# Kernel tuning notes

Measured on AMD Instinct MI355X. Metric: run time of the kernel, lower is better.

Reference implementation:

```python
import jax, jax.numpy as jnp
import numpy as np

TOTAL = 16384
IN_DIM = 512
OUT_DIM = 512
HEADS = 8
NUM_GRAPHS = 16


def setup_inputs() -> dict:
    key = jax.random.key(0)
    ks = jax.random.split(key, 8)
    x = jax.random.normal(ks[0], (TOTAL, IN_DIM), dtype=jnp.float32)
    batch = jnp.sort(jax.random.randint(ks[1], (TOTAL,), 0, NUM_GRAPHS)).astype(jnp.int64)
    s = 0.02
    # torch nn.MultiheadAttention packed in-projection: [3E, E] weight, [3E] bias
    in_proj_w = jax.random.normal(ks[2], (3 * IN_DIM, IN_DIM), dtype=jnp.float32) * s
    in_proj_b = jnp.zeros((3 * IN_DIM,), dtype=jnp.float32)
    out_proj_w = jax.random.normal(ks[3], (IN_DIM, IN_DIM), dtype=jnp.float32) * s
    out_proj_b = jnp.zeros((IN_DIM,), dtype=jnp.float32)
    lin_w = jax.random.normal(ks[4], (OUT_DIM, IN_DIM), dtype=jnp.float32) * s
    lin_b = jnp.zeros((OUT_DIM,), dtype=jnp.float32)
    return {"x": x, "batch": batch, "in_proj_w": in_proj_w, "in_proj_b": in_proj_b,
            "out_proj_w": out_proj_w, "out_proj_b": out_proj_b,
            "lin_w": lin_w, "lin_b": lin_b}


def _dense_indices(batch):
    """Host-side computation of (B, max_len, pos) from the sorted segment ids."""
    b_np = np.asarray(batch)
    B = int(b_np.max()) + 1
    counts = np.bincount(b_np, minlength=B)
    max_len = int(counts.max())
    offsets = np.concatenate([[0], np.cumsum(counts)[:-1]])  # start of each graph
    pos = jnp.asarray(np.arange(b_np.shape[0]) - offsets[b_np])  # within-graph index
    return B, max_len, pos


def reference(x, batch, in_proj_w, in_proj_b, out_proj_w, out_proj_b, lin_w, lin_b):
    T, E = x.shape
    H = HEADS
    D = E // H
    B, N, pos = _dense_indices(batch)

    # to_dense_batch: scatter ragged tokens into [B, N, E] + boolean mask [B, N]
    x_dense = jnp.zeros((B, N, E), x.dtype).at[batch, pos].set(x)
    mask = jnp.zeros((B, N), bool).at[batch, pos].set(True)

    # packed in-projection (torch MultiheadAttention semantics)
    qkv = x_dense @ in_proj_w.T + in_proj_b            # [B, N, 3E]
    q, k, v = jnp.split(qkv, 3, axis=-1)
    q = q.reshape(B, N, H, D)
    k = k.reshape(B, N, H, D)
    v = v.reshape(B, N, H, D)

    scores = jnp.einsum('bqhd,bkhd->bhqk', q, k) / jnp.sqrt(jnp.float32(D))
    # key_padding_mask = ~mask: padded keys are excluded
    scores = jnp.where(mask[:, None, None, :], scores, -jnp.inf)
    attn = jax.nn.softmax(scores, axis=-1)             # [B, H, N, N]
    ctx = jnp.einsum('bhqk,bkhd->bqhd', attn, v).reshape(B, N, E)
    attn_out = ctx @ out_proj_w.T + out_proj_b         # [B, N, E]

    y_dense = attn_out @ lin_w.T + lin_b               # [B, N, OUT_DIM]
    # unpad: x_out = y_dense[mask] == gather at the same (batch, pos) indices
    return y_dense[batch, pos]
```

## Files before the change

### kernel.cpp

```cpp
#include <hip/hip_runtime.h>
#include <stdint.h>
#include <stddef.h>

typedef unsigned short u16;
typedef unsigned int u32;
typedef __bf16 bf16x8 __attribute__((ext_vector_type(8)));
typedef _Float16 f16x8 __attribute__((ext_vector_type(8)));
typedef float f32x4 __attribute__((ext_vector_type(4)));

#define TT 16384
#define NG 16
#define MAXT 160
#define SCL 0.18033688011112042f

static __device__ __forceinline__ unsigned f2bf_u(float f) {
  unsigned u = __float_as_uint(f);
  return (u + 0x7fffu + ((u >> 16) & 1u)) >> 16;
}

static __device__ __forceinline__ void gl_lds16(const u16* g, u16* l) {
  __builtin_amdgcn_global_load_lds(
      (const __attribute__((address_space(1))) u32*)g,
      (__attribute__((address_space(3))) u32*)l, 16, 0, 0);
}

template <int CTRL>
static __device__ __forceinline__ float dppf(float x) {
  return __int_as_float(__builtin_amdgcn_mov_dpp(__float_as_int(x), CTRL, 0xF, 0xF, true));
}

#define NXF4 2097152
#define NWQ4 65536

__global__ __launch_bounds__(256) void prep_wc_kernel(
    const float* __restrict__ x, const float* __restrict__ ipw,
    const int* __restrict__ batch, const float* __restrict__ ipb,
    u16* __restrict__ xb, u16* __restrict__ ipwb, float* __restrict__ bqk,
    int* __restrict__ seg,
    const float* __restrict__ Wl, const float* __restrict__ Wo,
    const float* __restrict__ bo, const float* __restrict__ bl,
    u16* __restrict__ Wc, float* __restrict__ bc) {
  const int tid = threadIdx.x;
  __shared__ float sWl[16][512];
  __shared__ float red[256];
  __shared__ int scnt[NG];
  if (blockIdx.x > 1120) {
    const int bw = blockIdx.x - 1121;
    const int r0 = (bw >> 2) << 4;
    const int c0 = (bw & 3) << 7;
    const int col = c0 + (tid & 127), rh = (tid >> 7) << 3;
    for (int i = tid; i < 16 * 512; i += 256)
      sWl[i >> 9][i & 511] = Wl[(r0 + (i >> 9)) * 512 + (i & 511)];
    __syncthreads();
    float a[8] = {};
#pragma unroll 4
    for (int k = 0; k < 512; ++k) {
      float w = Wo[k * 512 + col];
#pragma unroll
      for (int r = 0; r < 8; ++r) a[r] += sWl[rh + r][k] * w;
    }
#pragma unroll
    for (int r = 0; r < 8; ++r) Wc[(r0 + rh + r) * 512 + col] = (u16)f2bf_u(a[r]);
    if (c0 == 0) {
      for (int r = 0; r < 16; ++r) {
        float p = 0.f;
        for (int k = tid; k < 512; k += 256) p += sWl[r][k] * bo[k];
        red[tid] = p;
        __syncthreads();
        for (int st = 128; st > 0; st >>= 1) {
          if (tid < st) red[tid] += red[tid + st];
          __syncthreads();
        }
        if (tid == 0) bc[r0 + r] = red[0] + bl[r0 + r];
        __syncthreads();
      }
    }
    return;
  }
  if (blockIdx.x == 1120) {
    if (tid < NG) scnt[tid] = 0;
    __syncthreads();
    for (int i = tid; i < TT; i += 256) atomicAdd(&scnt[batch[i] & (NG - 1)], 1);
    for (int i = tid; i < 1024; i += 256) bqk[i] = ipb[i] * (i < 512 ? SCL : 1.f);
    __syncthreads();
    if (tid == 0) {
      int off = 0, nt = 0;
      for (int g = 0; g < NG; ++g) { seg[1 + g] = off; off += scnt[g]; }
      seg[1 + NG] = off;
      for (int g = 0; g < NG; ++g)
        for (int q0 = 0; q0 < scnt[g]; q0 += 128) { seg[32 + nt] = g; seg[320 + nt] = q0; ++nt; }
      seg[0] = nt;
    }
    return;
  }
  const int base = blockIdx.x * 2048 + tid;
#pragma unroll
  for (int u = 0; u < 8; ++u) {
    int j = base + u * 256;
    float4 f;
    if (j < NXF4) f = ((const float4*)x)[j];
    else          f = ((const float4*)ipw)[j - NXF4];
    if (j >= NXF4 && j < NXF4 + NWQ4) { f.x *= SCL; f.y *= SCL; f.z *= SCL; f.w *= SCL; }
    uint2 o;
    o.x = f2bf_u(f.x) | (f2bf_u(f.y) << 16);
    o.y = f2bf_u(f.z) | (f2bf_u(f.w) << 16);
    if (j < NXF4) ((uint2*)xb)[j] = o;
    else          ((uint2*)ipwb)[j - NXF4] = o;
  }
}

template <int EPI>
static __device__ __forceinline__ void gemm_core(
    u16* As, u16* Bs, int bidx,
    const u16* __restrict__ A, const u16* __restrict__ Bt, void* __restrict__ C,
    void* __restrict__ C2, const float* __restrict__ bias, int M, int N, int K) {
  const int nn = N >> 7;
  const int bm = bidx / nn, bn = bidx % nn;
  const int tid = threadIdx.x;
  const int w = tid >> 6, lane = tid & 63;
  const int quad = lane >> 4, l16 = lane & 15;
  const int wm = w >> 1, wn = w & 1;
  f32x4 acc[4][4];
#pragma unroll
  for (int mi = 0; mi < 4; ++mi)
#pragma unroll
    for (int ni = 0; ni < 4; ++ni) acc[mi][ni] = (f32x4){0.f, 0.f, 0.f, 0.f};
  const int sr = lane >> 3, scn = lane & 7;
  const int rowA0 = bm << 7, rowB0 = bn << 7;
  for (int kt = 0; kt < K; kt += 64) {
#pragma unroll
    for (int u = 0; u < 4; ++u) {
      int rbase = (w << 5) + (u << 3);
      int ml = rbase + sr;
      int ca = scn ^ (ml & 7);
      gl_lds16(A  + (size_t)(rowA0 + ml) * K + kt + ca * 8, As + (rbase << 6));
      gl_lds16(Bt + (size_t)(rowB0 + ml) * K + kt + ca * 8, Bs + (rbase << 6));
    }
    __syncthreads();
#pragma unroll
    for (int ks = 0; ks < 2; ++ks) {
      bf16x8 af[4], bfv[4];
#pragma unroll
      for (int mi = 0; mi < 4; ++mi) {
        int r = (wm << 6) + (mi << 4) + l16;
        af[mi] = *(const bf16x8*)(As + (r << 6) + ((((ks << 2) + quad) ^ (r & 7)) << 3));
      }
#pragma unroll
      for (int ni = 0; ni < 4; ++ni) {
        int r = (wn << 6) + (ni << 4) + l16;
        bfv[ni] = *(const bf16x8*)(Bs + (r << 6) + ((((ks << 2) + quad) ^ (r & 7)) << 3));
      }
#pragma unroll
      for (int mi = 0; mi < 4; ++mi)
#pragma unroll
        for (int ni = 0; ni < 4; ++ni)
          acc[mi][ni] = __builtin_amdgcn_mfma_f32_16x16x32_bf16(af[mi], bfv[ni], acc[mi][ni], 0, 0, 0);
    }
    __syncthreads();
  }
#pragma unroll
  for (int mi = 0; mi < 4; ++mi) {
#pragma unroll
    for (int ni = 0; ni < 4; ++ni) {
      int row = rowA0 + (wm << 6) + (mi << 4) + (quad << 2);
      int col = rowB0 + (wn << 6) + (ni << 4) + l16;
      float bvc = (EPI == 2) ? 0.f : bias[col];
#pragma unroll
      for (int r = 0; r < 4; ++r) {
        float v = acc[mi][ni][r] + ((EPI == 2) ? bias[row + r] : bvc);
        if (EPI == 0) {
          ((float*)C)[(size_t)(row + r) * N + col] = v;
        } else if (EPI == 1) {
          if (col < 512) {
            ((u16*)C)[(size_t)(row + r) * 512 + col] = (u16)f2bf_u(v);
          } else {
            int f = col - 512, hh = f >> 6, d = f & 63, t = row + r;
            ((u16*)C2)[(size_t)hh * (TT * 64) + ((t >> 6) << 12) + ((t & 63) << 6) + d] = (u16)f2bf_u(v);
          }
        } else {
          int f = row + r, hh = f >> 6, d = f & 63, t = col;
          ((u16*)C)[(size_t)hh * (TT * 64) + ((t >> 6) << 12) + (d << 6) + (t & 63)] =
              __builtin_bit_cast(unsigned short, (_Float16)v);
        }
      }
    }
  }
}

__global__ __launch_bounds__(256) void gemm_qkv(
    const u16* __restrict__ xb, const u16* __restrict__ ipwb,
    u16* __restrict__ qb, u16* __restrict__ kpk, u16* __restrict__ vpk,
    const float* __restrict__ bqk, const float* __restrict__ ipb) {
  __shared__ __align__(16) u16 As[128 * 64];
  __shared__ __align__(16) u16 Bs[128 * 64];
  if (blockIdx.x < 1024)
    gemm_core<1>(As, Bs, blockIdx.x, xb, ipwb, qb, kpk, bqk, TT, 1024, 512);
  else
    gemm_core<2>(As, Bs, blockIdx.x - 1024, ipwb + 1024 * 512, xb, vpk, nullptr,
                 ipb + 1024, 512, TT, 512);
}

__global__ __launch_bounds__(256) void gemm_out(
    const u16* __restrict__ ctxb, const u16* __restrict__ wcb,
    float* __restrict__ out, const float* __restrict__ bc) {
  __shared__ __align__(16) u16 As[128 * 64];
  __shared__ __align__(16) u16 Bs[128 * 64];
  gemm_core<0>(As, Bs, blockIdx.x, ctxb, wcb, out, nullptr, bc, TT, 512, 512);
}

__global__ __launch_bounds__(512, 4) void attn_kernel(
    const u16* __restrict__ qb, const u16* __restrict__ kpk,
    const u16* __restrict__ vpk, u16* __restrict__ ctx, const int* __restrict__ seg) {
  const int bx = blockIdx.x;
  if (bx >= seg[0]) return;
  const int h = blockIdx.y;
  const int g = seg[32 + bx], q0 = seg[320 + bx];
  const int s0 = seg[1 + g], len = seg[2 + g] - s0;
  const int tid = threadIdx.x, w = tid >> 6, lane = tid & 63;
  const int quad = lane >> 4, l16 = lane & 15;

  __shared__ __align__(16) u16 Ks[2][4096];
  __shared__ __align__(16) u16 Vs[2][4096];
  __shared__ __align__(16) u16 Ps[8192];

  const u16* kh = kpk + (size_t)h * (TT * 64);
  const u16* vh = vpk + (size_t)h * (TT * 64);

  bf16x8 afq[2];
#pragma unroll
  for (int ks = 0; ks < 2; ++ks) {
    int ql = (w << 4) + l16;
    uint4 tmp = {0u, 0u, 0u, 0u};
    if (q0 + ql < len)
      tmp = *(const uint4*)(qb + (size_t)(s0 + q0 + ql) * 512 + (h << 6) + (((ks << 2) + quad) << 3));
    afq[ks] = __builtin_bit_cast(bf16x8, tmp);
  }

  f32x4 lrow = (f32x4){0.f, 0.f, 0.f, 0.f};
  f32x4 O[4];
#pragma unroll
  for (int dt = 0; dt < 4; ++dt) O[dt] = (f32x4){0.f, 0.f, 0.f, 0.f};

  const int delta = s0 & 7;
  const int srl = lane >> 3, sc = lane & 7;
  int vcl = ((len - 8 + delta) & ~7) - delta;
  if (vcl < -delta) vcl = -delta;

  const int rb = (w << 3);
  const int r0 = rb + srl;
  const int ca0 = sc ^ (r0 & 7);
  const int t0 = s0 - delta;
  int tk = t0 + r0;
  u32 kOffA = ((tk >> 6) << 12) + ((tk & 63) << 6) + (ca0 << 3);
  int tv = t0 + (ca0 << 3);
  u32 vOffA = ((tv >> 6) << 12) + (r0 << 6) + (tv & 63);

  auto stage = [&](int kv0, u16* bk, u16* bvs) {
    if (kv0 + 64 <= len) {
      gl_lds16(kh + kOffA, bk + (rb << 6));
      gl_lds16(vh + vOffA, bvs + (rb << 6));
    } else {
      int tr = kv0 + r0; tr = tr < len - 1 ? tr : len - 1; int tc = s0 + tr;
      gl_lds16(kh + ((tc >> 6) << 12) + ((tc & 63) << 6) + (ca0 << 3), bk + (rb << 6));
      int st = kv0 + (ca0 << 3); st = st < len ? st : vcl; tc = s0 + st;
      gl_lds16(vh + ((tc >> 6) << 12) + (r0 << 6) + (tc & 63), bvs + (rb << 6));
    }
    kOffA += 4096; vOffA += 4096;
  };

  const int nIt = (len + delta + 63) >> 6;
  u16* Pw = Ps + (w << 10);

  auto body = [&](int kv0, int i, const u16* Kc, const u16* Vc, u16* Kn, u16* Vn) {
    __syncthreads();
    if (i + 1 < nIt) stage(kv0 + 64, Kn, Vn);

    f32x4 s[4];
#pragma unroll
    for (int nt = 0; nt < 4; ++nt) s[nt] = (f32x4){0.f, 0.f, 0.f, 0.f};
#pragma unroll
    for (int ks = 0; ks < 2; ++ks) {
#pragma unroll
      for (int nt = 0; nt < 4; ++nt) {
        int kr = (nt << 4) + l16;
        bf16x8 bk = *(const bf16x8*)(Kc + (kr << 6) + ((((ks << 2) + quad) ^ (kr & 7)) << 3));
        s[nt] = __builtin_amdgcn_mfma_f32_16x16x32_bf16(afq[ks], bk, s[nt], 0, 0, 0);
      }
    }
    if ((kv0 < 0) | (kv0 + 64 > len)) {
#pragma unroll
      for (int nt = 0; nt < 4; ++nt) {
        int ki = kv0 + (nt << 4) + l16;
        float msk = ((unsigned)ki < (unsigned)len) ? 0.f : -1e30f;
#pragma unroll
        for (int r = 0; r < 4; ++r) s[nt][r] += msk;
      }
    }
#pragma unroll
    for (int nt = 0; nt < 4; ++nt)
#pragma unroll
      for (int r = 0; r < 4; ++r) s[nt][r] = __builtin_amdgcn_exp2f(s[nt][r]);
#pragma unroll
    for (int r = 0; r < 4; ++r)
      lrow[r] += (s[0][r] + s[1][r]) + (s[2][r] + s[3][r]);
#pragma unroll
    for (int nt = 0; nt < 4; ++nt)
#pragma unroll
      for (int r = 0; r < 4; ++r) {
        float a = s[nt][r];
        float b = dppf<0xB1>(a);
        if (!(l16 & 1)) {
          u32 p = __builtin_bit_cast(u32, __builtin_amdgcn_cvt_pkrtz(a, b));
          int prow = (quad << 2) + r, kc = (nt << 4) + l16;
          *(u32*)(Pw + (prow << 6) + (((kc >> 3) ^ (prow & 7)) << 3) + (kc & 7)) = p;
        }
      }
#pragma unroll
    for (int ks = 0; ks < 2; ++ks) {
      f16x8 ap = *(const f16x8*)(Pw + (l16 << 6) + ((((ks << 2) + quad) ^ (l16 & 7)) << 3));
#pragma unroll
      for (int dt = 0; dt < 4; ++dt) {
        int vr = (dt << 4) + l16;
        f16x8 bv = *(const f16x8*)(Vc + (vr << 6) + ((((ks << 2) + quad) ^ (vr & 7)) << 3));
        O[dt] = __builtin_amdgcn_mfma_f32_16x16x32_f16(ap, bv, O[dt], 0, 0, 0);
      }
    }
  };

  stage(-delta, Ks[0], Vs[0]);
  {
    int kv0 = -delta, i = 0;
    while (i < nIt) {
      body(kv0, i, Ks[0], Vs[0], Ks[1], Vs[1]);
      ++i; kv0 += 64;
      if (i >= nIt) break;
      body(kv0, i, Ks[1], Vs[1], Ks[0], Vs[0]);
      ++i; kv0 += 64;
    }
  }

  {
    f32x4 inv;
#pragma unroll
    for (int r = 0; r < 4; ++r) {
      float t = lrow[r];
      t += dppf<0xB1>(t);
      t += dppf<0x4E>(t);
      t += dppf<0x124>(t);
      t += dppf<0x128>(t);
      inv[r] = 1.f / t;
    }
#pragma unroll
    for (int dt = 0; dt < 4; ++dt)
#pragma unroll
      for (int r = 0; r < 4; ++r) {
        int ql = (w << 4) + (quad << 2) + r;
        if (q0 + ql < len)
          ctx[(size_t)(s0 + q0 + ql) * 512 + (h << 6) + (dt << 4) + l16] = (u16)f2bf_u(O[dt][r] * inv[r]);
      }
  }
}

extern "C" void kernel_launch(void* const* d_in, const int* in_sizes, int n_in,
                              void* d_out, int out_size, void* d_ws, size_t ws_size,
                              hipStream_t stream) {
  const float* x = (const float*)d_in[0];
  const int* batch = (const int*)d_in[1];
  const float* ipw = (const float*)d_in[2];
  const float* ipb = (const float*)d_in[3];
  const float* opw = (const float*)d_in[4];
  const float* opb = (const float*)d_in[5];
  const float* lw = (const float*)d_in[6];
  const float* lb = (const float*)d_in[7];
  float* out = (float*)d_out;
  char* ws = (char*)d_ws;

  u16* xb   = (u16*)(ws + 0);
  u16* ctxb = (u16*)(ws + 0);
  u16* qb   = (u16*)(ws + 16777216);
  u16* kpk  = (u16*)(ws + 33554432);
  u16* vpk  = (u16*)(ws + 50331648);
  u16* ipwb = (u16*)(ws + 67108864);
  u16* wcb  = (u16*)(ws + 68681728);
  float* bc = (float*)(ws + 69206016);
  float* bqk= (float*)(ws + 69208064);
  int* seg  = (int*)(ws + 69212160);

  prep_wc_kernel<<<1249, 256, 0, stream>>>(x, ipw, batch, ipb, xb, ipwb, bqk, seg,
                                           lw, opw, opb, lb, wcb, bc);
  gemm_qkv<<<1536, 256, 0, stream>>>(xb, ipwb, qb, kpk, vpk, bqk, ipb);
  attn_kernel<<<dim3(MAXT, 8), 512, 0, stream>>>(qb, kpk, vpk, ctxb, seg);
  gemm_out<<<512, 256, 0, stream>>>(ctxb, wcb, out, bc);
  (void)in_sizes; (void)n_in; (void)out_size; (void)ws_size;
}
```

Measured before the change: 281.2 us.

## Halve attention query tile to 64 rows with 256-thread blocks and MFMA priority

Each attention block now covers 64 query rows with 4 waves instead of 128 rows with 8 waves, so the tile list and grid roughly double. Each thread issues two K and two V LDS loads per stage to keep the 64-key tile fully staged, and the P buffer is halved. s_setprio is raised around the MFMA loops to favour matrix issue across waves. The intent is better CU occupancy and less wasted padding on the ragged tail tiles, at the cost of loading each K/V tile twice as often overall.

After: 269.8 us. -4.0%, faster.

```diff
diff --git a/kernel.cpp b/kernel.cpp
--- a/kernel.cpp
+++ b/kernel.cpp
@@ -10,7 +10,7 @@
 
 #define TT 16384
 #define NG 16
-#define MAXT 160
+#define MAXT 272
 #define SCL 0.18033688011112042f
 
 static __device__ __forceinline__ unsigned f2bf_u(float f) {
@@ -88,7 +88,7 @@
       for (int g = 0; g < NG; ++g) { seg[1 + g] = off; off += scnt[g]; }
       seg[1 + NG] = off;
       for (int g = 0; g < NG; ++g)
-        for (int q0 = 0; q0 < scnt[g]; q0 += 128) { seg[32 + nt] = g; seg[320 + nt] = q0; ++nt; }
+        for (int q0 = 0; q0 < scnt[g]; q0 += 64) { seg[32 + nt] = g; seg[320 + nt] = q0; ++nt; }
       seg[0] = nt;
     }
     return;
@@ -208,7 +208,7 @@
   gemm_core<0>(As, Bs, blockIdx.x, ctxb, wcb, out, nullptr, bc, TT, 512, 512);
 }
 
-__global__ __launch_bounds__(512, 4) void attn_kernel(
+__global__ __launch_bounds__(256, 4) void attn_kernel(
     const u16* __restrict__ qb, const u16* __restrict__ kpk,
     const u16* __restrict__ vpk, u16* __restrict__ ctx, const int* __restrict__ seg) {
   const int bx = blockIdx.x;
@@ -221,7 +221,7 @@
 
   __shared__ __align__(16) u16 Ks[2][4096];
   __shared__ __align__(16) u16 Vs[2][4096];
-  __shared__ __align__(16) u16 Ps[8192];
+  __shared__ __align__(16) u16 Ps[4096];
 
   const u16* kh = kpk + (size_t)h * (TT * 64);
   const u16* vh = vpk + (size_t)h * (TT * 64);
@@ -246,26 +246,36 @@
   int vcl = ((len - 8 + delta) & ~7) - delta;
   if (vcl < -delta) vcl = -delta;
 
-  const int rb = (w << 3);
-  const int r0 = rb + srl;
-  const int ca0 = sc ^ (r0 & 7);
+  const int rb0 = (w << 4), rb1 = rb0 + 8;
+  const int r0 = rb0 + srl, r1 = rb1 + srl;
+  const int ca0 = sc ^ (r0 & 7), ca1 = sc ^ (r1 & 7);
   const int t0 = s0 - delta;
   int tk = t0 + r0;
   u32 kOffA = ((tk >> 6) << 12) + ((tk & 63) << 6) + (ca0 << 3);
+  tk = t0 + r1;
+  u32 kOffB = ((tk >> 6) << 12) + ((tk & 63) << 6) + (ca1 << 3);
   int tv = t0 + (ca0 << 3);
   u32 vOffA = ((tv >> 6) << 12) + (r0 << 6) + (tv & 63);
+  tv = t0 + (ca1 << 3);
+  u32 vOffB = ((tv >> 6) << 12) + (r1 << 6) + (tv & 63);
 
   auto stage = [&](int kv0, u16* bk, u16* bvs) {
     if (kv0 + 64 <= len) {
-      gl_lds16(kh + kOffA, bk + (rb << 6));
-      gl_lds16(vh + vOffA, bvs + (rb << 6));
+      gl_lds16(kh + kOffA, bk + (rb0 << 6));
+      gl_lds16(kh + kOffB, bk + (rb1 << 6));
+      gl_lds16(vh + vOffA, bvs + (rb0 << 6));
+      gl_lds16(vh + vOffB, bvs + (rb1 << 6));
     } else {
       int tr = kv0 + r0; tr = tr < len - 1 ? tr : len - 1; int tc = s0 + tr;
-      gl_lds16(kh + ((tc >> 6) << 12) + ((tc & 63) << 6) + (ca0 << 3), bk + (rb << 6));
+      gl_lds16(kh + ((tc >> 6) << 12) + ((tc & 63) << 6) + (ca0 << 3), bk + (rb0 << 6));
+      tr = kv0 + r1; tr = tr < len - 1 ? tr : len - 1; tc = s0 + tr;
+      gl_lds16(kh + ((tc >> 6) << 12) + ((tc & 63) << 6) + (ca1 << 3), bk + (rb1 << 6));
       int st = kv0 + (ca0 << 3); st = st < len ? st : vcl; tc = s0 + st;
-      gl_lds16(vh + ((tc >> 6) << 12) + (r0 << 6) + (tc & 63), bvs + (rb << 6));
-    }
-    kOffA += 4096; vOffA += 4096;
+      gl_lds16(vh + ((tc >> 6) << 12) + (r0 << 6) + (tc & 63), bvs + (rb0 << 6));
+      st = kv0 + (ca1 << 3); st = st < len ? st : vcl; tc = s0 + st;
+      gl_lds16(vh + ((tc >> 6) << 12) + (r1 << 6) + (tc & 63), bvs + (rb1 << 6));
+    }
+    kOffA += 4096; kOffB += 4096; vOffA += 4096; vOffB += 4096;
   };
 
   const int nIt = (len + delta + 63) >> 6;
@@ -278,6 +288,7 @@
     f32x4 s[4];
 #pragma unroll
     for (int nt = 0; nt < 4; ++nt) s[nt] = (f32x4){0.f, 0.f, 0.f, 0.f};
+    __builtin_amdgcn_s_setprio(1);
 #pragma unroll
     for (int ks = 0; ks < 2; ++ks) {
 #pragma unroll
@@ -287,6 +298,7 @@
         s[nt] = __builtin_amdgcn_mfma_f32_16x16x32_bf16(afq[ks], bk, s[nt], 0, 0, 0);
       }
     }
+    __builtin_amdgcn_s_setprio(0);
     if ((kv0 < 0) | (kv0 + 64 > len)) {
 #pragma unroll
       for (int nt = 0; nt < 4; ++nt) {
@@ -318,12 +330,14 @@
 #pragma unroll
     for (int ks = 0; ks < 2; ++ks) {
       f16x8 ap = *(const f16x8*)(Pw + (l16 << 6) + ((((ks << 2) + quad) ^ (l16 & 7)) << 3));
+      __builtin_amdgcn_s_setprio(1);
 #pragma unroll
       for (int dt = 0; dt < 4; ++dt) {
         int vr = (dt << 4) + l16;
         f16x8 bv = *(const f16x8*)(Vc + (vr << 6) + ((((ks << 2) + quad) ^ (vr & 7)) << 3));
         O[dt] = __builtin_amdgcn_mfma_f32_16x16x32_f16(ap, bv, O[dt], 0, 0, 0);
       }
+      __builtin_amdgcn_s_setprio(0);
     }
   };
 
@@ -389,7 +403,7 @@
   prep_wc_kernel<<<1249, 256, 0, stream>>>(x, ipw, batch, ipb, xb, ipwb, bqk, seg,
                                            lw, opw, opb, lb, wcb, bc);
   gemm_qkv<<<1536, 256, 0, stream>>>(xb, ipwb, qb, kpk, vpk, bqk, ipb);
-  attn_kernel<<<dim3(MAXT, 8), 512, 0, stream>>>(qb, kpk, vpk, ctxb, seg);
+  attn_kernel<<<dim3(MAXT, 8), 256, 0, stream>>>(qb, kpk, vpk, ctxb, seg);
   gemm_out<<<512, 256, 0, stream>>>(ctxb, wcb, out, bc);
   (void)in_sizes; (void)n_in; (void)out_size; (void)ws_size;
 }
```
